# Kernel tuning notes

Measured on AMD Instinct MI355X. Metric: run time of the kernel, lower is better.

## Reference

```python
import jax, jax.numpy as jnp
import numpy as np

EPS = 1e-12  # torch F.normalize eps


def setup_inputs() -> dict:
    key = jax.random.key(0)
    ks = jax.random.split(key, 6)
    N, D, F = 32768, 512, 64
    return {
        "x1": jax.random.normal(ks[0], (N, D), dtype=jnp.float32),
        "x2": jax.random.normal(ks[1], (1, D), dtype=jnp.float32),
        "V": jax.random.normal(ks[2], (F, 2 * D), dtype=jnp.float32),
        "W": jax.random.normal(ks[3], (F, D, D), dtype=jnp.float32),
        "b": jax.random.normal(ks[4], (F,), dtype=jnp.float32),
        "U": jax.random.normal(ks[5], (F, 1), dtype=jnp.float32),
    }


def reference(x1, x2, V, W, b, U):
    D = x1.shape[1]
    # V term: concat(x1, tile(x2)) @ V[i] for all i -> split V into the x1 and x2 halves
    V1, V2 = V[:, :D], V[:, D:]          # (F, D) each
    v_out = x1 @ V1.T + x2 @ V2.T        # (N, F) + (1, F) broadcast
    # W term: x1 @ W[i] @ x2^T for all i, as one batched bilinear contraction
    w_out = jnp.einsum('nd,fde,e->nf', x1, W, x2[0])  # (N, F)
    fm = v_out + w_out + b               # (N, F)
    # L1 normalize along dim=1 (torch F.normalize semantics)
    denom = jnp.maximum(jnp.sum(jnp.abs(fm), axis=1, keepdims=True), EPS)
    out = jax.nn.relu(fm / denom)
    return out @ U                       # (N, 1)
```

## Files before the change

### kernel.cpp

```cpp
#include <hip/hip_runtime.h>
#include <hip/hip_bf16.h>
#include <stdint.h>

#define NROWS 32768
#define DDIM  512
#define FDIM  64

typedef __attribute__((ext_vector_type(4))) float f32x4;
typedef __attribute__((ext_vector_type(8))) short bf16x8;

static __device__ __forceinline__ unsigned short f2bf_rne(float x) {
    unsigned u = __builtin_bit_cast(unsigned, x);
    u += 0x7fffu + ((u >> 16) & 1u);
    return (unsigned short)(u >> 16);
}
static __device__ __forceinline__ unsigned pack2_bf16(float a, float b) {
    unsigned ua = __builtin_bit_cast(unsigned, a);
    unsigned ub = __builtin_bit_cast(unsigned, b);
    ua += 0x7fffu + ((ua >> 16) & 1u);
    ub += 0x7fffu + ((ub >> 16) & 1u);
    return (ua >> 16) | (ub & 0xffff0000u);
}

static __device__ __forceinline__ void async_copy16(const void* g, void* l) {
    __builtin_amdgcn_global_load_lds(
        (const __attribute__((address_space(1))) unsigned int*)g,
        (__attribute__((address_space(3))) unsigned int*)l,
        16, 0, 0);
}

__global__ __launch_bounds__(256) void prep_kernel(
    const float* __restrict__ x2,
    const float* __restrict__ V,
    const float* __restrict__ W,
    const float* __restrict__ b,
    unsigned short* __restrict__ Mout,
    float* __restrict__ cout)
{
    int wave = (blockIdx.x * 256 + threadIdx.x) >> 6;
    int lane = threadIdx.x & 63;

    const float4* src;
    if (wave < FDIM * DDIM) {
        src = (const float4*)(W + (size_t)wave * DDIM);
    } else {
        int f = wave - FDIM * DDIM;
        src = (const float4*)(V + (size_t)f * (2 * DDIM) + DDIM);
    }
    const float4* xx = (const float4*)x2;

    float4 a0 = src[lane];
    float4 a1 = src[lane + 64];
    float4 x0 = xx[lane];
    float4 x1v = xx[lane + 64];

    float s = a0.x * x0.x + a0.y * x0.y + a0.z * x0.z + a0.w * x0.w
            + a1.x * x1v.x + a1.y * x1v.y + a1.z * x1v.z + a1.w * x1v.w;

    #pragma unroll
    for (int m = 32; m >= 1; m >>= 1) s += __shfl_xor(s, m);

    if (lane == 0) {
        if (wave < FDIM * DDIM) {
            int f = wave >> 9, d = wave & 511;
            float mval = s + V[(size_t)f * (2 * DDIM) + d];
            int t  = f >> 4, fl = f & 15;
            int ks = d >> 5, sub = (d >> 3) & 3, j = d & 7;
            int fragidx = (((ks * 4 + t) * 64 + sub * 16 + fl) << 3) + j;
            Mout[fragidx] = f2bf_rne(mval);
        } else {
            int f = wave - FDIM * DDIM;
            cout[f] = s + b[f];
        }
    }
}

__global__ __launch_bounds__(256, 2) void main_kernel(
    const float* __restrict__ x1,
    const unsigned short* __restrict__ Mg,
    const float* __restrict__ cg,
    const float* __restrict__ U,
    float* __restrict__ out)
{
    __shared__ uint4 Mlds[4096];

    int tid  = threadIdx.x;
    int wave = tid >> 6;
    int lane = tid & 63;

    const uint4* Msrc = (const uint4*)Mg;
    #pragma unroll
    for (int it = 0; it < 16; ++it) {
        int base = it * 256 + wave * 64;
        async_copy16(Msrc + base + lane, &Mlds[base]);
    }
    __syncthreads();

    int q  = lane >> 4;
    int fl = lane & 15;

    int row0 = blockIdx.x * 64 + wave * 16;
    const float* arow = x1 + (size_t)(row0 + fl) * DDIM + q * 8;

    const bf16x8* Mf = (const bf16x8*)Mlds;

    f32x4 acc0 = {0.f,0.f,0.f,0.f}, acc1 = {0.f,0.f,0.f,0.f};
    f32x4 acc2 = {0.f,0.f,0.f,0.f}, acc3 = {0.f,0.f,0.f,0.f};

    #pragma unroll 4
    for (int ks = 0; ks < 16; ++ks) {
        float4 av0 = *(const float4*)(arow + ks * 32);
        float4 av1 = *(const float4*)(arow + ks * 32 + 4);

        union { bf16x8 v; unsigned u32[4]; } af;
        af.u32[0] = pack2_bf16(av0.x, av0.y);
        af.u32[1] = pack2_bf16(av0.z, av0.w);
        af.u32[2] = pack2_bf16(av1.x, av1.y);
        af.u32[3] = pack2_bf16(av1.z, av1.w);

        bf16x8 b0 = Mf[(ks * 4 + 0) * 64 + lane];
        bf16x8 b1 = Mf[(ks * 4 + 1) * 64 + lane];
        bf16x8 b2 = Mf[(ks * 4 + 2) * 64 + lane];
        bf16x8 b3 = Mf[(ks * 4 + 3) * 64 + lane];

        acc0 = __builtin_amdgcn_mfma_f32_16x16x32_bf16(af.v, b0, acc0, 0, 0, 0);
        acc1 = __builtin_amdgcn_mfma_f32_16x16x32_bf16(af.v, b1, acc1, 0, 0, 0);
        acc2 = __builtin_amdgcn_mfma_f32_16x16x32_bf16(af.v, b2, acc2, 0, 0, 0);
        acc3 = __builtin_amdgcn_mfma_f32_16x16x32_bf16(af.v, b3, acc3, 0, 0, 0);
    }

    float cf0 = cg[fl], cf1 = cg[16 + fl], cf2 = cg[32 + fl], cf3 = cg[48 + fl];
    float uf0 = U[fl],  uf1 = U[16 + fl],  uf2 = U[32 + fl],  uf3 = U[48 + fl];

    #pragma unroll
    for (int r = 0; r < 4; ++r) {
        float f0 = acc0[r] + cf0;
        float f1 = acc1[r] + cf1;
        float f2 = acc2[r] + cf2;
        float f3 = acc3[r] + cf3;

        float s = fabsf(f0) + fabsf(f1) + fabsf(f2) + fabsf(f3);
        s += __shfl_xor(s, 1); s += __shfl_xor(s, 2);
        s += __shfl_xor(s, 4); s += __shfl_xor(s, 8);
        float denom = fmaxf(s, 1e-12f);

        float o = fmaxf(f0, 0.f) * uf0 + fmaxf(f1, 0.f) * uf1
                + fmaxf(f2, 0.f) * uf2 + fmaxf(f3, 0.f) * uf3;
        o += __shfl_xor(o, 1); o += __shfl_xor(o, 2);
        o += __shfl_xor(o, 4); o += __shfl_xor(o, 8);

        if (fl == 0) {
            out[row0 + q * 4 + r] = o / denom;
        }
    }
}

extern "C" void kernel_launch(void* const* d_in, const int* in_sizes, int n_in,
                              void* d_out, int out_size, void* d_ws, size_t ws_size,
                              hipStream_t stream) {
    const float* x1 = (const float*)d_in[0];
    const float* x2 = (const float*)d_in[1];
    const float* V  = (const float*)d_in[2];
    const float* W  = (const float*)d_in[3];
    const float* b  = (const float*)d_in[4];
    const float* U  = (const float*)d_in[5];
    float* outp = (float*)d_out;

    unsigned short* M = (unsigned short*)d_ws;
    float* c          = (float*)((char*)d_ws + FDIM * DDIM * 2);

    prep_kernel<<<8208, 256, 0, stream>>>(x2, V, W, b, M, c);
    main_kernel<<<512, 256, 0, stream>>>(x1, M, c, U, outp);
}
```

Measured before the change: 152.2 us.

## Fuse prep and main kernels into one cooperative kernel with grid sync

Combines the W·x2 reduction prep stage and the MFMA main stage into a single cooperative launch of 512 blocks, separated by a grid-wide barrier. Each wave now handles 16 W rows with register double-buffered loads instead of one row per wave, which cuts the 8208-block launch and the inter-kernel gap. The cost is a grid sync and lower prep parallelism, since only 2048 waves stream 64 MB of W. The old two-kernel path stays as a fallback if the cooperative launch fails.

```diff
diff --git a/kernel.cpp b/kernel.cpp
--- a/kernel.cpp
+++ b/kernel.cpp
@@ -1,6 +1,8 @@
 #include <hip/hip_runtime.h>
-#include <hip/hip_bf16.h>
+#include <hip/hip_cooperative_groups.h>
 #include <stdint.h>
+
+namespace cg = cooperative_groups;
 
 #define NROWS 32768
 #define DDIM  512
@@ -27,6 +29,156 @@
         (const __attribute__((address_space(1))) unsigned int*)g,
         (__attribute__((address_space(3))) unsigned int*)l,
         16, 0, 0);
+}
+
+static __device__ __forceinline__ float dot8(const float4 a0, const float4 a1,
+                                             const float4 x0, const float4 x1v) {
+    return a0.x * x0.x + a0.y * x0.y + a0.z * x0.z + a0.w * x0.w
+         + a1.x * x1v.x + a1.y * x1v.y + a1.z * x1v.z + a1.w * x1v.w;
+}
+
+__global__ __launch_bounds__(256, 2) void fused_kernel(
+    const float* __restrict__ x1,
+    const float* __restrict__ x2,
+    const float* __restrict__ V,
+    const float* __restrict__ W,
+    const float* __restrict__ b,
+    const float* __restrict__ U,
+    unsigned short* __restrict__ Mg,
+    float* __restrict__ cg_,
+    float* __restrict__ out)
+{
+    __shared__ uint4 Mlds[4096];
+
+    int tid  = threadIdx.x;
+    int wave = tid >> 6;
+    int lane = tid & 63;
+    int gw   = blockIdx.x * 4 + wave;
+
+    const float4* xx = (const float4*)x2;
+    float4 x0  = xx[lane];
+    float4 x1v = xx[lane + 64];
+
+    float4 ca[4][2], na[4][2];
+
+    #pragma unroll
+    for (int i = 0; i < 4; ++i) {
+        int r = gw + i * 2048;
+        const float4* src = (const float4*)(W + (size_t)r * DDIM);
+        ca[i][0] = src[lane];
+        ca[i][1] = src[lane + 64];
+    }
+
+    #pragma unroll
+    for (int k = 0; k < 4; ++k) {
+        if (k < 3) {
+            #pragma unroll
+            for (int i = 0; i < 4; ++i) {
+                int r = gw + ((k + 1) * 4 + i) * 2048;
+                const float4* src = (const float4*)(W + (size_t)r * DDIM);
+                na[i][0] = src[lane];
+                na[i][1] = src[lane + 64];
+            }
+        }
+        #pragma unroll
+        for (int i = 0; i < 4; ++i) {
+            int r = gw + (k * 4 + i) * 2048;
+            float s = dot8(ca[i][0], ca[i][1], x0, x1v);
+            #pragma unroll
+            for (int m = 32; m >= 1; m >>= 1) s += __shfl_xor(s, m);
+            if (lane == 0) {
+                int f = r >> 9, d = r & 511;
+                float mval = s + V[(size_t)f * (2 * DDIM) + d];
+                int t  = f >> 4, fl2 = f & 15;
+                int ks = d >> 5, sub = (d >> 3) & 3, j = d & 7;
+                int fragidx = (((ks * 4 + t) * 64 + sub * 16 + fl2) << 3) + j;
+                Mg[fragidx] = f2bf_rne(mval);
+            }
+        }
+        if (k < 3) {
+            #pragma unroll
+            for (int i = 0; i < 4; ++i) { ca[i][0] = na[i][0]; ca[i][1] = na[i][1]; }
+        }
+    }
+
+    if (gw < FDIM) {
+        const float4* src = (const float4*)(V + (size_t)gw * (2 * DDIM) + DDIM);
+        float4 a0 = src[lane], a1 = src[lane + 64];
+        float s = dot8(a0, a1, x0, x1v);
+        #pragma unroll
+        for (int m = 32; m >= 1; m >>= 1) s += __shfl_xor(s, m);
+        if (lane == 0) cg_[gw] = s + b[gw];
+    }
+
+    __threadfence();
+    cg::this_grid().sync();
+    __threadfence();
+
+    const uint4* Msrc = (const uint4*)Mg;
+    #pragma unroll
+    for (int it = 0; it < 16; ++it) {
+        int base = it * 256 + wave * 64;
+        async_copy16(Msrc + base + lane, &Mlds[base]);
+    }
+    __syncthreads();
+
+    int q  = lane >> 4;
+    int fl = lane & 15;
+
+    int row0 = blockIdx.x * 64 + wave * 16;
+    const float* arow = x1 + (size_t)(row0 + fl) * DDIM + q * 8;
+
+    const bf16x8* Mf = (const bf16x8*)Mlds;
+
+    f32x4 acc0 = {0.f,0.f,0.f,0.f}, acc1 = {0.f,0.f,0.f,0.f};
+    f32x4 acc2 = {0.f,0.f,0.f,0.f}, acc3 = {0.f,0.f,0.f,0.f};
+
+    #pragma unroll 4
+    for (int ks = 0; ks < 16; ++ks) {
+        float4 av0 = *(const float4*)(arow + ks * 32);
+        float4 av1 = *(const float4*)(arow + ks * 32 + 4);
+
+        union { bf16x8 v; unsigned u32[4]; } af;
+        af.u32[0] = pack2_bf16(av0.x, av0.y);
+        af.u32[1] = pack2_bf16(av0.z, av0.w);
+        af.u32[2] = pack2_bf16(av1.x, av1.y);
+        af.u32[3] = pack2_bf16(av1.z, av1.w);
+
+        bf16x8 b0 = Mf[(ks * 4 + 0) * 64 + lane];
+        bf16x8 b1 = Mf[(ks * 4 + 1) * 64 + lane];
+        bf16x8 b2 = Mf[(ks * 4 + 2) * 64 + lane];
+        bf16x8 b3 = Mf[(ks * 4 + 3) * 64 + lane];
+
+        acc0 = __builtin_amdgcn_mfma_f32_16x16x32_bf16(af.v, b0, acc0, 0, 0, 0);
+        acc1 = __builtin_amdgcn_mfma_f32_16x16x32_bf16(af.v, b1, acc1, 0, 0, 0);
+        acc2 = __builtin_amdgcn_mfma_f32_16x16x32_bf16(af.v, b2, acc2, 0, 0, 0);
+        acc3 = __builtin_amdgcn_mfma_f32_16x16x32_bf16(af.v, b3, acc3, 0, 0, 0);
+    }
+
+    float cf0 = cg_[fl], cf1 = cg_[16 + fl], cf2 = cg_[32 + fl], cf3 = cg_[48 + fl];
+    float uf0 = U[fl],   uf1 = U[16 + fl],  uf2 = U[32 + fl],  uf3 = U[48 + fl];
+
+    #pragma unroll
+    for (int r = 0; r < 4; ++r) {
+        float f0 = acc0[r] + cf0;
+        float f1 = acc1[r] + cf1;
+        float f2 = acc2[r] + cf2;
+        float f3 = acc3[r] + cf3;
+
+        float s = fabsf(f0) + fabsf(f1) + fabsf(f2) + fabsf(f3);
+        s += __shfl_xor(s, 1); s += __shfl_xor(s, 2);
+        s += __shfl_xor(s, 4); s += __shfl_xor(s, 8);
+        float denom = fmaxf(s, 1e-12f);
+
+        float o = fmaxf(f0, 0.f) * uf0 + fmaxf(f1, 0.f) * uf1
+                + fmaxf(f2, 0.f) * uf2 + fmaxf(f3, 0.f) * uf3;
+        o += __shfl_xor(o, 1); o += __shfl_xor(o, 2);
+        o += __shfl_xor(o, 4); o += __shfl_xor(o, 8);
+
+        if (fl == 0) {
+            out[row0 + q * 4 + r] = o / denom;
+        }
+    }
 }
 
 __global__ __launch_bounds__(256) void prep_kernel(
@@ -54,8 +206,7 @@
     float4 x0 = xx[lane];
     float4 x1v = xx[lane + 64];
 
-    float s = a0.x * x0.x + a0.y * x0.y + a0.z * x0.z + a0.w * x0.w
-            + a1.x * x1v.x + a1.y * x1v.y + a1.z * x1v.z + a1.w * x1v.w;
+    float s = dot8(a0, a1, x0, x1v);
 
     #pragma unroll
     for (int m = 32; m >= 1; m >>= 1) s += __shfl_xor(s, m);
@@ -78,7 +229,7 @@
 __global__ __launch_bounds__(256, 2) void main_kernel(
     const float* __restrict__ x1,
     const unsigned short* __restrict__ Mg,
-    const float* __restrict__ cg,
+    const float* __restrict__ cg_,
     const float* __restrict__ U,
     float* __restrict__ out)
 {
@@ -129,8 +280,8 @@
         acc3 = __builtin_amdgcn_mfma_f32_16x16x32_bf16(af.v, b3, acc3, 0, 0, 0);
     }
 
-    float cf0 = cg[fl], cf1 = cg[16 + fl], cf2 = cg[32 + fl], cf3 = cg[48 + fl];
-    float uf0 = U[fl],  uf1 = U[16 + fl],  uf2 = U[32 + fl],  uf3 = U[48 + fl];
+    float cf0 = cg_[fl], cf1 = cg_[16 + fl], cf2 = cg_[32 + fl], cf3 = cg_[48 + fl];
+    float uf0 = U[fl],   uf1 = U[16 + fl],  uf2 = U[32 + fl],  uf3 = U[48 + fl];
 
     #pragma unroll
     for (int r = 0; r < 4; ++r) {
@@ -169,6 +320,12 @@
     unsigned short* M = (unsigned short*)d_ws;
     float* c          = (float*)((char*)d_ws + FDIM * DDIM * 2);
 
-    prep_kernel<<<8208, 256, 0, stream>>>(x2, V, W, b, M, c);
-    main_kernel<<<512, 256, 0, stream>>>(x1, M, c, U, outp);
-}
+    void* kargs[] = { (void*)&x1, (void*)&x2, (void*)&V, (void*)&W, (void*)&b,
+                      (void*)&U,  (void*)&M,  (void*)&c, (void*)&outp };
+    hipError_t e = hipLaunchCooperativeKernel((const void*)fused_kernel,
+                                              dim3(512), dim3(256), kargs, 0, stream);
+    if (e != hipSuccess) {
+        prep_kernel<<<8208, 256, 0, stream>>>(x2, V, W, b, M, c);
+        main_kernel<<<512, 256, 0, stream>>>(x1, M, c, U, outp);
+    }
+}
```

Result: slower. 276.4 us (+81.6%).

## Split K across wave pairs and read folded weights from global instead of LDS

Applied to the files above, without the earlier changes.

The main kernel now assigns each 16-row tile to two waves, each covering half of the 512-wide reduction, and combines their partial accumulators through a small LDS buffer. It launches twice as many blocks of 32 rows each. It also drops the bulk async staging of the 64 KB bf16 weight matrix into LDS and reads B fragments directly from global/L2. The goal is more parallelism and occupancy on a memory-bound x1 stream, at the cost of repeated global reads of the weights and an extra barrier.

```diff
diff --git a/kernel.cpp b/kernel.cpp
--- a/kernel.cpp
+++ b/kernel.cpp
@@ -1,5 +1,4 @@
 #include <hip/hip_runtime.h>
-#include <hip/hip_bf16.h>
 #include <stdint.h>
 
 #define NROWS 32768
@@ -22,11 +21,10 @@
     return (ua >> 16) | (ub & 0xffff0000u);
 }
 
-static __device__ __forceinline__ void async_copy16(const void* g, void* l) {
-    __builtin_amdgcn_global_load_lds(
-        (const __attribute__((address_space(1))) unsigned int*)g,
-        (__attribute__((address_space(3))) unsigned int*)l,
-        16, 0, 0);
+static __device__ __forceinline__ float dot8(const float4 a0, const float4 a1,
+                                             const float4 x0, const float4 x1v) {
+    return a0.x * x0.x + a0.y * x0.y + a0.z * x0.z + a0.w * x0.w
+         + a1.x * x1v.x + a1.y * x1v.y + a1.z * x1v.z + a1.w * x1v.w;
 }
 
 __global__ __launch_bounds__(256) void prep_kernel(
@@ -54,8 +52,7 @@
     float4 x0 = xx[lane];
     float4 x1v = xx[lane + 64];
 
-    float s = a0.x * x0.x + a0.y * x0.y + a0.z * x0.z + a0.w * x0.w
-            + a1.x * x1v.x + a1.y * x1v.y + a1.z * x1v.z + a1.w * x1v.w;
+    float s = dot8(a0, a1, x0, x1v);
 
     #pragma unroll
     for (int m = 32; m >= 1; m >>= 1) s += __shfl_xor(s, m);
@@ -75,40 +72,35 @@
     }
 }
 
-__global__ __launch_bounds__(256, 2) void main_kernel(
+__global__ __launch_bounds__(256) void main_kernel(
     const float* __restrict__ x1,
     const unsigned short* __restrict__ Mg,
-    const float* __restrict__ cg,
+    const float* __restrict__ cg_,
     const float* __restrict__ U,
     float* __restrict__ out)
 {
-    __shared__ uint4 Mlds[4096];
+    __shared__ f32x4 red[2][64][4];
 
-    int tid  = threadIdx.x;
-    int wave = tid >> 6;
-    int lane = tid & 63;
-
-    const uint4* Msrc = (const uint4*)Mg;
-    #pragma unroll
-    for (int it = 0; it < 16; ++it) {
-        int base = it * 256 + wave * 64;
-        async_copy16(Msrc + base + lane, &Mlds[base]);
-    }
-    __syncthreads();
+    int tid   = threadIdx.x;
+    int wave  = tid >> 6;
+    int lane  = tid & 63;
+    int tile  = wave >> 1;
+    int khalf = wave & 1;
 
     int q  = lane >> 4;
     int fl = lane & 15;
 
-    int row0 = blockIdx.x * 64 + wave * 16;
-    const float* arow = x1 + (size_t)(row0 + fl) * DDIM + q * 8;
+    int row0 = blockIdx.x * 32 + tile * 16;
+    const float* arow = x1 + (size_t)(row0 + fl) * DDIM + q * 8 + khalf * 256;
 
-    const bf16x8* Mf = (const bf16x8*)Mlds;
+    const bf16x8* Mf = (const bf16x8*)Mg;
 
     f32x4 acc0 = {0.f,0.f,0.f,0.f}, acc1 = {0.f,0.f,0.f,0.f};
     f32x4 acc2 = {0.f,0.f,0.f,0.f}, acc3 = {0.f,0.f,0.f,0.f};
 
     #pragma unroll 4
-    for (int ks = 0; ks < 16; ++ks) {
+    for (int ks = 0; ks < 8; ++ks) {
+        int ksg = khalf * 8 + ks;
         float4 av0 = *(const float4*)(arow + ks * 32);
         float4 av1 = *(const float4*)(arow + ks * 32 + 4);
 
@@ -118,10 +110,10 @@
         af.u32[2] = pack2_bf16(av1.x, av1.y);
         af.u32[3] = pack2_bf16(av1.z, av1.w);
 
-        bf16x8 b0 = Mf[(ks * 4 + 0) * 64 + lane];
-        bf16x8 b1 = Mf[(ks * 4 + 1) * 64 + lane];
-        bf16x8 b2 = Mf[(ks * 4 + 2) * 64 + lane];
-        bf16x8 b3 = Mf[(ks * 4 + 3) * 64 + lane];
+        bf16x8 b0 = Mf[(ksg * 4 + 0) * 64 + lane];
+        bf16x8 b1 = Mf[(ksg * 4 + 1) * 64 + lane];
+        bf16x8 b2 = Mf[(ksg * 4 + 2) * 64 + lane];
+        bf16x8 b3 = Mf[(ksg * 4 + 3) * 64 + lane];
 
         acc0 = __builtin_amdgcn_mfma_f32_16x16x32_bf16(af.v, b0, acc0, 0, 0, 0);
         acc1 = __builtin_amdgcn_mfma_f32_16x16x32_bf16(af.v, b1, acc1, 0, 0, 0);
@@ -129,8 +121,22 @@
         acc3 = __builtin_amdgcn_mfma_f32_16x16x32_bf16(af.v, b3, acc3, 0, 0, 0);
     }
 
-    float cf0 = cg[fl], cf1 = cg[16 + fl], cf2 = cg[32 + fl], cf3 = cg[48 + fl];
-    float uf0 = U[fl],  uf1 = U[16 + fl],  uf2 = U[32 + fl],  uf3 = U[48 + fl];
+    if (khalf == 1) {
+        red[tile][lane][0] = acc0;
+        red[tile][lane][1] = acc1;
+        red[tile][lane][2] = acc2;
+        red[tile][lane][3] = acc3;
+    }
+    __syncthreads();
+    if (khalf == 1) return;
+
+    acc0 += red[tile][lane][0];
+    acc1 += red[tile][lane][1];
+    acc2 += red[tile][lane][2];
+    acc3 += red[tile][lane][3];
+
+    float cf0 = cg_[fl], cf1 = cg_[16 + fl], cf2 = cg_[32 + fl], cf3 = cg_[48 + fl];
+    float uf0 = U[fl],   uf1 = U[16 + fl],  uf2 = U[32 + fl],  uf3 = U[48 + fl];
 
     #pragma unroll
     for (int r = 0; r < 4; ++r) {
@@ -170,5 +176,5 @@
     float* c          = (float*)((char*)d_ws + FDIM * DDIM * 2);
 
     prep_kernel<<<8208, 256, 0, stream>>>(x2, V, W, b, M, c);
-    main_kernel<<<512, 256, 0, stream>>>(x1, M, c, U, outp);
+    main_kernel<<<1024, 256, 0, stream>>>(x1, M, c, U, outp);
 }
```

Measured after the change: 153.2 us. About the same (+0.7%).
